# Performance work log

Hardware: AMD Instinct MI355X
Metric: run time of the kernel (lower is better)

Reference implementation:

```python
import jax, jax.numpy as jnp
import numpy as np

N = 60000      # nodes
E = 240000     # edges
H = 256        # hidden_channels
M = 64         # middle_channels
F1 = 12        # num_radial * num_spherical**2
F2 = 6         # num_radial * num_spherical
L = 4          # num_layers (InterBlocks)
NL = 3         # num_output_layers (residual linears per block)
G = 2000       # number of graphs in batch
EPS = 1e-5


def setup_inputs() -> dict:
    key = jax.random.key(0)
    ks = iter(jax.random.split(key, 64))
    def nrm(shape, scale=0.05):
        return jax.random.normal(next(ks), shape, jnp.float32) * scale
    inp = {
        'x_idx': jax.random.randint(next(ks), (N, 9), 0, 178, jnp.int32),
        'edge_attr_idx': jax.random.randint(next(ks), (E, 3), 0, 18, jnp.int32),
        'edge_index': jax.random.randint(next(ks), (2, E), 0, N, jnp.int32),
        'batch': jnp.sort(jax.random.randint(next(ks), (N,), 0, G, jnp.int32)),
        'feature1': jax.random.uniform(next(ks), (E, F1), jnp.float32),
        'feature2': jax.random.uniform(next(ks), (E, F2), jnp.float32),
        # embeddings
        'x_tab': nrm((178, H)), 'e_tab': nrm((18, H)),
        # lin_x: Linear + BN + ReLU
        'linx_w': nrm((L, H, H)), 'linx_b': jnp.zeros((L, H)), 'linx_g': jnp.ones((L, H)), 'linx_be': jnp.zeros((L, H)),
        # lin_feat1: Linear(F1,M) + BN(M) + ReLU + Linear(M,H) + ReLU
        'f1_w1': nrm((L, F1, M)), 'f1_b1': jnp.zeros((L, M)), 'f1_g': jnp.ones((L, M)), 'f1_be': jnp.zeros((L, M)),
        'f1_w2': nrm((L, M, H)), 'f1_b2': jnp.zeros((L, H)),
        # lin_feat2: Linear(F2,M) + BN(M) + ReLU + Linear(M,H) + ReLU
        'f2_w1': nrm((L, F2, M)), 'f2_b1': jnp.zeros((L, M)), 'f2_g': jnp.ones((L, M)), 'f2_be': jnp.zeros((L, M)),
        'f2_w2': nrm((L, M, H)), 'f2_b2': jnp.zeros((L, H)),
        # EdgeGraphConv 1 & 2 (PyG GraphConv: lin_rel(aggr) + lin_root(x), root has no bias)
        'c1_rel_w': nrm((L, H, H)), 'c1_rel_b': jnp.zeros((L, H)), 'c1_root_w': nrm((L, H, H)),
        'c2_rel_w': nrm((L, H, H)), 'c2_rel_b': jnp.zeros((L, H)), 'c2_root_w': nrm((L, H, H)),
        # lin_cat
        'cat_w': nrm((L, 2 * H, H)), 'cat_b': jnp.zeros((L, H)),
        # residual linears
        'lins_w': nrm((L, NL, H, H)), 'lins_b': jnp.zeros((L, NL, H)),
        # GraphNorm
        'gn_w': jnp.ones((L, H)), 'gn_b': jnp.zeros((L, H)), 'gn_ms': jnp.ones((L, H)),
        # final
        'fin_w': nrm((L, H, H)), 'fin_b': jnp.zeros((L, H)),
    }
    return inp


def _bn(h, g, b):
    m = h.mean(0)
    v = jnp.mean((h - m) ** 2, axis=0)
    return (h - m) * jax.lax.rsqrt(v + EPS) * g + b


def _conv(x, src, dst, ew, rel_w, rel_b, root_w):
    # EdgeGraphConv: message = x_j * edge_weight, sum-aggregate at dst
    msg = x[src] * ew                                   # [E, H]
    agg = jax.ops.segment_sum(msg, dst, num_segments=N)  # [N, H]
    return agg @ rel_w + rel_b + x @ root_w


def _graphnorm(h, batch, w, b, ms):
    cnt = jnp.maximum(jax.ops.segment_sum(jnp.ones((h.shape[0], 1), h.dtype), batch, num_segments=G), 1.0)
    mean = jax.ops.segment_sum(h, batch, num_segments=G) / cnt
    out = h - ms * mean[batch]
    var = jax.ops.segment_sum(out ** 2, batch, num_segments=G) / cnt
    return out * jax.lax.rsqrt(var[batch] + EPS) * w + b


def reference(x_idx, edge_attr_idx, edge_index, batch, feature1, feature2, x_tab, e_tab,
              linx_w, linx_b, linx_g, linx_be,
              f1_w1, f1_b1, f1_g, f1_be, f1_w2, f1_b2,
              f2_w1, f2_b1, f2_g, f2_be, f2_w2, f2_b2,
              c1_rel_w, c1_rel_b, c1_root_w, c2_rel_w, c2_rel_b, c2_root_w,
              cat_w, cat_b, lins_w, lins_b, gn_w, gn_b, gn_ms, fin_w, fin_b):
    relu = jax.nn.relu
    x = x_tab[x_idx].sum(1)                 # [N, H] atom-feature embedding sum
    _e = e_tab[edge_attr_idx].sum(1)        # edge embedding (computed, unused downstream as in source)
    src, dst = edge_index[0], edge_index[1]
    for l in range(L):
        xl = relu(_bn(x @ linx_w[l] + linx_b[l], linx_g[l], linx_be[l]))
        w1 = relu(relu(_bn(feature1 @ f1_w1[l] + f1_b1[l], f1_g[l], f1_be[l])) @ f1_w2[l] + f1_b2[l])
        w2 = relu(relu(_bn(feature2 @ f2_w1[l] + f2_b1[l], f2_g[l], f2_be[l])) @ f2_w2[l] + f2_b2[l])
        h1 = relu(_conv(xl, src, dst, w1, c1_rel_w[l], c1_rel_b[l], c1_root_w[l]))
        h2 = relu(_conv(xl, src, dst, w2, c2_rel_w[l], c2_rel_b[l], c2_root_w[l]))
        h = relu(jnp.concatenate([h1, h2], axis=1) @ cat_w[l] + cat_b[l])
        h = h + xl
        for k in range(NL):
            h = relu(h @ lins_w[l, k] + lins_b[l, k]) + h
        h = _graphnorm(h, batch, gn_w[l], gn_b[l], gn_ms[l])
        x = h @ fin_w[l] + fin_b[l]
    return x
```

## Files before the change

kernel.cpp:

```cpp
#include <hip/hip_runtime.h>
#include <cstdint>

constexpr int Nn = 60000;
constexpr int Ee = 240000;
constexpr int Hh = 256;
constexpr int Mm = 64;
constexpr int F1c = 12;
constexpr int Lc = 4;
constexpr int NLc = 3;
constexpr int Gc = 2000;
constexpr float EPSc = 1e-5f;
constexpr int NB = (Nn + 255) / 256;
constexpr int CSB = 256;

typedef _Float16 f16x8 __attribute__((ext_vector_type(8)));
typedef __attribute__((ext_vector_type(4))) float f32x4;
typedef __attribute__((ext_vector_type(4))) unsigned short u16x4;
typedef unsigned short ushortt;

__device__ __forceinline__ ushortt f2h(float f) {
    union { _Float16 h; ushortt u; } c; c.h = (_Float16)f; return c.u;
}
__device__ __forceinline__ float h2f(ushortt u) {
    union { _Float16 h; ushortt u; } c; c.u = u; return (float)c.h;
}

__global__ void embed_x_kernel(const int* __restrict__ xidx, const float* __restrict__ xtab,
                               ushortt* __restrict__ x) {
    int n = blockIdx.x;
    int c = threadIdx.x;
    __shared__ int idx[9];
    if (c < 9) idx[c] = xidx[n * 9 + c];
    __syncthreads();
    float s = 0.f;
#pragma unroll
    for (int j = 0; j < 9; j++) s += xtab[idx[j] * Hh + c];
    x[(size_t)n * Hh + c] = f2h(s);
}

__global__ void seg_bounds_kernel(const int* __restrict__ batch, int* __restrict__ gstart) {
    int g = blockIdx.x * 256 + threadIdx.x;
    if (g > Gc) return;
    if (g == Gc) { gstart[Gc] = Nn; return; }
    int lo = 0, hi = Nn;
    while (lo < hi) { int mid = (lo + hi) >> 1; if (batch[mid] < g) lo = mid + 1; else hi = mid; }
    gstart[g] = lo;
}

__global__ void deg_hist_kernel(const int* __restrict__ ei, int* __restrict__ deg) {
    int e = blockIdx.x * 256 + threadIdx.x;
    if (e >= Ee) return;
    atomicAdd(&deg[ei[Ee + e]], 1);
}

__global__ void psum_block_kernel(const int* __restrict__ deg, int* __restrict__ iscan,
                                  int* __restrict__ bsum) {
    __shared__ int s[256];
    int t = threadIdx.x;
    int i = blockIdx.x * 256 + t;
    int v = (i < Nn) ? deg[i] : 0;
    s[t] = v;
    __syncthreads();
    for (int off = 1; off < 256; off <<= 1) {
        int add = (t >= off) ? s[t - off] : 0;
        __syncthreads();
        s[t] += add;
        __syncthreads();
    }
    if (i < Nn) iscan[i] = s[t];
    if (t == 255) bsum[blockIdx.x] = s[255];
}

__global__ void scan_bsum_kernel(const int* __restrict__ bsum, int* __restrict__ ebase,
                                 int* __restrict__ rowptr) {
    if (threadIdx.x != 0 || blockIdx.x != 0) return;
    int run = 0;
    for (int b = 0; b < NB; b++) { ebase[b] = run; run += bsum[b]; }
    rowptr[Nn] = Ee;
}

__global__ void finalize_rowptr_kernel(const int* __restrict__ deg, const int* __restrict__ iscan,
                                       const int* __restrict__ ebase, int* __restrict__ rowptr) {
    int i = blockIdx.x * 256 + threadIdx.x;
    if (i >= Nn) return;
    rowptr[i] = ebase[i >> 8] + iscan[i] - deg[i];
}

__global__ void fill_eid_kernel(const int* __restrict__ ei, int* __restrict__ cursor,
                                int* __restrict__ eid, int* __restrict__ esrc) {
    int e = blockIdx.x * 256 + threadIdx.x;
    if (e >= Ee) return;
    int dst = ei[Ee + e];
    int pos = atomicAdd(&cursor[dst], 1);
    eid[pos] = e;
    esrc[pos] = ei[e];
}

template<int K>
__global__ void gather_feat_kernel(const float* __restrict__ F, const int* __restrict__ eid,
                                   ushortt* __restrict__ featS) {
    long i = (long)blockIdx.x * 256 + threadIdx.x;
    if (i >= (long)Ee * K) return;
    int e = (int)(i / K);
    int k = (int)(i % K);
    featS[i] = f2h(F[(size_t)eid[e] * K + k]);
}

__global__ void wconv_kernel(const float* __restrict__ src, ushortt* __restrict__ dst,
                             int nmat, int K, long dstMS, int kOff, long srcMS) {
    long idx = (long)blockIdx.x * 256 + threadIdx.x;
    long tot = (long)nmat * 256 * K;
    if (idx >= tot) return;
    int k = (int)(idx % K);
    long t = idx / K;
    int c = (int)(t & 255);
    int m = (int)(t >> 8);
    float w = src[m * srcMS + (long)k * 256 + c];
    int kg = kOff + k;
    int ks = kg >> 5;
    int k5 = kg & 31;
    int kpp = (((k5 & 15) >> 2) << 3) + (((k5 >> 4) & 1) << 2) + (k5 & 3);
    long o = m * dstMS + ((long)ks * 256 + c) * 32 + kpp;
    dst[o] = f2h(w);
}

template<int K>
__global__ void gram_kernel(const float* __restrict__ F, float* __restrict__ G,
                            float* __restrict__ s) {
    constexpr int NP = K * (K + 1) / 2;
    __shared__ float Ft[256 * K];
    int tid = threadIdx.x;
    int pi = 0, pj = 0;
    if (tid < NP) {
        int tt = tid;
        for (pi = 0; pi < K; pi++) { if (tt <= pi) { pj = tt; break; } tt -= (pi + 1); }
    }
    float acc = 0.f;
    int ntiles = (Ee + 255) / 256;
    for (int tile = blockIdx.x; tile < ntiles; tile += gridDim.x) {
        long r0 = (long)tile * 256;
        for (int idx = tid; idx < 256 * K; idx += 256) {
            long r = r0 + idx / K;
            Ft[idx] = (r < Ee) ? F[r * K + idx % K] : 0.f;
        }
        __syncthreads();
        if (tid < NP) {
            for (int r = 0; r < 256; r++) acc += Ft[r * K + pi] * Ft[r * K + pj];
        } else if (tid < NP + K) {
            int i = tid - NP;
            for (int r = 0; r < 256; r++) acc += Ft[r * K + i];
        }
        __syncthreads();
    }
    if (tid < NP) {
        atomicAdd(&G[pi * K + pj], acc);
        if (pi != pj) atomicAdd(&G[pj * K + pi], acc);
    } else if (tid < NP + K) {
        atomicAdd(&s[tid - NP], acc);
    }
}

__global__ void edge_bnparams_kernel(
    const float* __restrict__ G1, const float* __restrict__ s1,
    const float* __restrict__ G2, const float* __restrict__ s2,
    const float* __restrict__ f1_w1, const float* __restrict__ f1_b1,
    const float* __restrict__ f1_g, const float* __restrict__ f1_be,
    const float* __restrict__ f2_w1, const float* __restrict__ f2_b1,
    const float* __restrict__ f2_g, const float* __restrict__ f2_be,
    float Ecnt, float* __restrict__ scsAll, float* __restrict__ shsAll) {
    int lb = blockIdx.x;
    int l = lb >> 1, br = lb & 1;
    int m = threadIdx.x;
    const float* G = br ? G2 : G1;
    const float* sv = br ? s2 : s1;
    int K = br ? 6 : F1c;
    const float* W  = br ? (f2_w1 + (size_t)l * 6 * Mm)   : (f1_w1 + (size_t)l * F1c * Mm);
    const float* bb = br ? (f2_b1 + l * Mm) : (f1_b1 + l * Mm);
    const float* gg = br ? (f2_g + l * Mm)  : (f1_g + l * Mm);
    const float* be = br ? (f2_be + l * Mm) : (f1_be + l * Mm);
    float wm[F1c];
    for (int i = 0; i < K; i++) wm[i] = W[i * Mm + m];
    float sw = 0.f;
    for (int i = 0; i < K; i++) sw += sv[i] * wm[i];
    float q = 0.f;
    for (int i = 0; i < K; i++) {
        float gi = 0.f;
        for (int j = 0; j < K; j++) gi += G[i * K + j] * wm[j];
        q += wm[i] * gi;
    }
    float rinv = 1.f / Ecnt;
    float colsum = sw + Ecnt * bb[m];
    float colsq = q + 2.f * bb[m] * sw + Ecnt * bb[m] * bb[m];
    float mu = colsum * rinv;
    float var = colsq * rinv - mu * mu;
    float rs = rsqrtf(var + EPSc) * gg[m];
    scsAll[lb * 64 + m] = rs;
    shsAll[lb * 64 + m] = bb[m] * rs + be[m] - mu * rs;
}

__global__ void colstats_part_kernel(const ushortt* __restrict__ A, long tot4,
                                     float* __restrict__ part) {
    __shared__ float ls[1024], lq[1024];
    int tid = threadIdx.x;
    long i0 = (long)blockIdx.x * 256 + tid;
    long stride = (long)gridDim.x * 256;
    float s[4] = {0, 0, 0, 0}, q[4] = {0, 0, 0, 0};
    for (long i = i0; i < tot4; i += stride) {
        u16x4 v = *(const u16x4*)(A + i * 4);
#pragma unroll
        for (int j = 0; j < 4; j++) { float f = h2f(v[j]); s[j] += f; q[j] += f * f; }
    }
#pragma unroll
    for (int j = 0; j < 4; j++) { ls[tid * 4 + j] = s[j]; lq[tid * 4 + j] = q[j]; }
    __syncthreads();
    if (tid < 64) {
#pragma unroll
        for (int j = 0; j < 4; j++) {
            float ts = ls[tid * 4 + j] + ls[(tid + 64) * 4 + j] +
                       ls[(tid + 128) * 4 + j] + ls[(tid + 192) * 4 + j];
            float tq = lq[tid * 4 + j] + lq[(tid + 64) * 4 + j] +
                       lq[(tid + 128) * 4 + j] + lq[(tid + 192) * 4 + j];
            part[(size_t)blockIdx.x * 512 + tid * 4 + j] = ts;
            part[(size_t)blockIdx.x * 512 + 256 + tid * 4 + j] = tq;
        }
    }
}

__global__ void colstats_reduce_kernel(const float* __restrict__ part,
                                       float* __restrict__ colsum, float* __restrict__ colsq) {
    int t = blockIdx.x * 256 + threadIdx.x;
    float acc = 0.f;
    for (int b = 0; b < CSB; b++) acc += part[(size_t)b * 512 + t];
    if (t < 256) colsum[t] = acc;
    else colsq[t - 256] = acc;
}

__global__ void bn_relu_h_kernel(const ushortt* __restrict__ A, ushortt* __restrict__ outp,
                                 const float* __restrict__ sum, const float* __restrict__ sq,
                                 const float* __restrict__ g, const float* __restrict__ be,
                                 float rinv, long tot4) {
    long i = (long)blockIdx.x * 256 + threadIdx.x;
    if (i >= tot4) return;
    int c0 = (int)((i * 4) & 255);
    u16x4 v = *(const u16x4*)(A + i * 4);
    u16x4 o;
#pragma unroll
    for (int j = 0; j < 4; j++) {
        int c = c0 + j;
        float m = sum[c] * rinv;
        float var = sq[c] * rinv - m * m;
        float f = (h2f(v[j]) - m) * rsqrtf(var + EPSc) * g[c] + be[c];
        o[j] = f2h(fmaxf(f, 0.f));
    }
    *(u16x4*)(outp + i * 4) = o;
}

__global__ __launch_bounds__(256, 4) void bgemm_kernel(
    const void* __restrict__ A1v, int lda1, const ushortt* __restrict__ A2, int lda2,
    const ushortt* __restrict__ Wt,
    const float* __restrict__ bias, const ushortt* __restrict__ res,
    float* __restrict__ Cf, ushortt* __restrict__ Ch,
    int rows, int K1, int Ktot, int do_relu, int a1f32) {
    __shared__ char As[2][128 * 80];
    int tid = threadIdx.x;
    int lane = tid & 63;
    int wave = tid >> 6;
    int wrow0 = (wave >> 1) * 64;
    int wcol0 = (wave & 1) * 64;
    int r0 = blockIdx.y * 128;
    int j0 = blockIdx.x * 128;
    int l15 = lane & 15;
    int l4 = lane >> 4;

    int srow[4], sk4[4], soff[4];
#pragma unroll
    for (int p = 0; p < 4; p++) {
        int fid = p * 256 + tid;
        srow[p] = fid >> 3;
        sk4[p] = (fid & 7) * 4;
        soff[p] = srow[p] * 80 + ((((sk4[p] & 15) >> 2) << 4) + ((sk4[p] >> 4) << 3));
    }

    f32x4 acc[4][4];
#pragma unroll
    for (int i = 0; i < 4; i++)
#pragma unroll
        for (int j = 0; j < 4; j++) acc[i][j] = (f32x4){0.f, 0.f, 0.f, 0.f};

    for (int kt = 0; kt < Ktot; kt += 64) {
        const void* Av; int lda; int koff; int f32;
        if (kt < K1) { Av = A1v; lda = lda1; koff = kt; f32 = a1f32; }
        else         { Av = (const void*)A2; lda = lda2; koff = kt - K1; f32 = 0; }

        u16x4 hv[2][4];
        if (f32) {
#pragma unroll
            for (int h = 0; h < 2; h++)
#pragma unroll
                for (int p = 0; p < 4; p++) {
                    int rg = r0 + srow[p]; if (rg >= rows) rg = rows - 1;
                    float4 v = *(const float4*)((const float*)Av +
                        (size_t)rg * lda + koff + h * 32 + sk4[p]);
                    u16x4 hh;
                    hh[0] = f2h(v.x); hh[1] = f2h(v.y); hh[2] = f2h(v.z); hh[3] = f2h(v.w);
                    hv[h][p] = hh;
                }
        } else {
#pragma unroll
            for (int h = 0; h < 2; h++)
#pragma unroll
                for (int p = 0; p < 4; p++) {
                    int rg = r0 + srow[p]; if (rg >= rows) rg = rows - 1;
                    hv[h][p] = *(const u16x4*)((const ushortt*)Av +
                        (size_t)rg * lda + koff + h * 32 + sk4[p]);
                }
        }
        f16x8 bh[2][4];
#pragma unroll
        for (int h = 0; h < 2; h++) {
            long kb = ((long)((kt + h * 32) >> 5) * 256) * 32;
#pragma unroll
            for (int j = 0; j < 4; j++) {
                int colrow = j0 + wcol0 + j * 16 + l15;
                bh[h][j] = *(const f16x8*)(Wt + kb + (long)colrow * 32 + l4 * 8);
            }
        }
#pragma unroll
        for (int h = 0; h < 2; h++)
#pragma unroll
            for (int p = 0; p < 4; p++) *(u16x4*)(As[h] + soff[p]) = hv[h][p];
        __syncthreads();

#pragma unroll
        for (int h = 0; h < 2; h++) {
            f16x8 ah[4];
#pragma unroll
            for (int i = 0; i < 4; i++) {
                int row = wrow0 + i * 16 + l15;
                ah[i] = *(const f16x8*)(As[h] + row * 80 + l4 * 16);
            }
#pragma unroll
            for (int i = 0; i < 4; i++)
#pragma unroll
                for (int j = 0; j < 4; j++)
                    acc[i][j] = __builtin_amdgcn_mfma_f32_16x16x32_f16(ah[i], bh[h][j], acc[i][j], 0, 0, 0);
        }
        __syncthreads();
    }

#pragma unroll
    for (int i = 0; i < 4; i++) {
#pragma unroll
        for (int r = 0; r < 4; r++) {
            int row = r0 + wrow0 + i * 16 + l4 * 4 + r;
            if (row >= rows) continue;
#pragma unroll
            for (int j = 0; j < 4; j++) {
                int col = j0 + wcol0 + j * 16 + l15;
                float v = acc[i][j][r] + bias[col];
                if (do_relu) v = fmaxf(v, 0.f);
                if (res) v += h2f(res[(size_t)row * 256 + col]);
                if (Cf) Cf[(size_t)row * 256 + col] = v;
                if (Ch) Ch[(size_t)row * 256 + col] = f2h(v);
            }
        }
    }
}

template<int K>
__global__ __launch_bounds__(256, 4) void edge_gemm_kernel(
    const ushortt* __restrict__ featS, const float* __restrict__ W1,
    const float* __restrict__ scs, const float* __restrict__ shs,
    const ushortt* __restrict__ Wt, const float* __restrict__ bias,
    ushortt* __restrict__ Wc, int c0, int ec) {
    constexpr int KP = K + 1;
    __shared__ char As[2][128 * 80];
    __shared__ float Fs[128 * KP];
    __shared__ float W1s[K * 64];
    __shared__ float scsS[64], shsS[64];
    int tid = threadIdx.x;
    for (int i = tid; i < K * 64; i += 256) W1s[i] = W1[i];
    if (tid < 64) { scsS[tid] = scs[tid]; shsS[tid] = shs[tid]; }
    int r0 = blockIdx.y * 128;
    for (int idx = tid; idx < 128 * K; idx += 256) {
        int row = idx / K;
        int k = idx % K;
        long e = (long)c0 + r0 + row;
        if (e >= Ee) e = Ee - 1;
        Fs[row * KP + k] = h2f(featS[e * K + k]);
    }
    __syncthreads();
    {
        int row = tid >> 1;
        int m0 = (tid & 1) * 32;
        const float* fr = &Fs[row * KP];
#pragma unroll
        for (int mm = 0; mm < 32; mm++) {
            int m = m0 + mm;
            float u = 0.f;
#pragma unroll
            for (int k = 0; k < K; k++) u += fr[k] * W1s[k * 64 + m];
            float v = fmaxf(u * scsS[m] + shsS[m], 0.f);
            int k5 = m & 31;
            int kpp = (((k5 & 15) >> 2) << 3) + (((k5 >> 4) & 1) << 2) + (k5 & 3);
            *(ushortt*)(As[m >> 5] + row * 80 + kpp * 2) = f2h(v);
        }
    }
    __syncthreads();

    int lane = tid & 63;
    int wave = tid >> 6;
    int wrow0 = (wave >> 1) * 64;
    int wcol0 = (wave & 1) * 64;
    int j0 = blockIdx.x * 128;
    int l15 = lane & 15;
    int l4 = lane >> 4;

    f32x4 acc[4][4];
#pragma unroll
    for (int i = 0; i < 4; i++)
#pragma unroll
        for (int j = 0; j < 4; j++) acc[i][j] = (f32x4){0.f, 0.f, 0.f, 0.f};

#pragma unroll
    for (int kt = 0; kt < 64; kt += 32) {
        f16x8 bh[4];
        long kb = ((long)(kt >> 5) * 256) * 32;
#pragma unroll
        for (int j = 0; j < 4; j++) {
            int colrow = j0 + wcol0 + j * 16 + l15;
            bh[j] = *(const f16x8*)(Wt + kb + (long)colrow * 32 + l4 * 8);
        }
        f16x8 ah[4];
        const char* Az = As[kt >> 5];
#pragma unroll
        for (int i = 0; i < 4; i++) {
            int row = wrow0 + i * 16 + l15;
            ah[i] = *(const f16x8*)(Az + row * 80 + l4 * 16);
        }
#pragma unroll
        for (int i = 0; i < 4; i++)
#pragma unroll
            for (int j = 0; j < 4; j++)
                acc[i][j] = __builtin_amdgcn_mfma_f32_16x16x32_f16(ah[i], bh[j], acc[i][j], 0, 0, 0);
    }

#pragma unroll
    for (int i = 0; i < 4; i++) {
#pragma unroll
        for (int r = 0; r < 4; r++) {
            int row = wrow0 + i * 16 + l4 * 4 + r;
            if (r0 + row >= ec) continue;
#pragma unroll
            for (int j = 0; j < 4; j++) {
                int col = j0 + wcol0 + j * 16 + l15;
                float v = fmaxf(acc[i][j][r] + bias[col], 0.f);
                Wc[(size_t)(r0 + row) * 256 + col] = f2h(v);
            }
        }
    }
}

__global__ __launch_bounds__(256) void gather_agg_kernel(
    const int* __restrict__ rowptr, const int* __restrict__ esrc,
    const ushortt* __restrict__ Wc, const ushortt* __restrict__ xl,
    float* __restrict__ agg, ushortt* __restrict__ out16, int c0, int c1, int first) {
    int n = (blockIdx.x * 256 + threadIdx.x) >> 6;
    if (n >= Nn) return;
    int lane = threadIdx.x & 63;
    int rs = rowptr[n], re = rowptr[n + 1];
    if (rs < c0) rs = c0;
    if (re > c1) re = c1;
    float4 acc;
    if (out16 || first) {
        acc = make_float4(0.f, 0.f, 0.f, 0.f);
    } else {
        if (rs >= re) return;
        acc = *(float4*)(agg + (size_t)n * Hh + lane * 4);
    }
    for (int i = rs; i < re; i++) {
        u16x4 wv = *(const u16x4*)(Wc + (size_t)(i - c0) * Hh + lane * 4);
        u16x4 xv = *(const u16x4*)(xl + (size_t)esrc[i] * Hh + lane * 4);
        acc.x += h2f(wv[0]) * h2f(xv[0]);
        acc.y += h2f(wv[1]) * h2f(xv[1]);
        acc.z += h2f(wv[2]) * h2f(xv[2]);
        acc.w += h2f(wv[3]) * h2f(xv[3]);
    }
    if (out16) {
        u16x4 o;
        o[0] = f2h(acc.x); o[1] = f2h(acc.y); o[2] = f2h(acc.z); o[3] = f2h(acc.w);
        *(u16x4*)(out16 + (size_t)n * Hh + lane * 4) = o;
    } else {
        *(float4*)(agg + (size_t)n * Hh + lane * 4) = acc;
    }
}

__global__ __launch_bounds__(256) void gn_fused_kernel(
    const ushortt* __restrict__ h, const int* __restrict__ gstart,
    const float* __restrict__ ms, const float* __restrict__ w, const float* __restrict__ b,
    ushortt* __restrict__ outp) {
    __shared__ ushortt seg[128 * 256];
    int g = blockIdx.x;
    int c = threadIdx.x;
    int s = gstart[g], e = gstart[g + 1];
    int cnt = e - s;
    float cntf = (float)(cnt > 1 ? cnt : 1);
    float msc = ms[c], wc = w[c], bc = b[c];
    if (cnt <= 128) {
        float acc = 0.f;
        for (int n = 0; n < cnt; n++) {
            ushortt v = h[(size_t)(s + n) * Hh + c];
            seg[n * 256 + c] = v;
            acc += h2f(v);
        }
        float mean = acc / cntf;
        float sq = 0.f;
        for (int n = 0; n < cnt; n++) {
            ushortt ho = f2h(h2f(seg[n * 256 + c]) - msc * mean);
            seg[n * 256 + c] = ho;
            float o2 = h2f(ho);
            sq += o2 * o2;
        }
        float rstd = rsqrtf(sq / cntf + EPSc);
        for (int n = 0; n < cnt; n++) {
            float ov = h2f(seg[n * 256 + c]);
            outp[(size_t)(s + n) * Hh + c] = f2h(ov * rstd * wc + bc);
        }
    } else {
        float acc = 0.f;
        for (int n = s; n < e; n++) acc += h2f(h[(size_t)n * Hh + c]);
        float mean = acc / cntf;
        float sq = 0.f;
        for (int n = s; n < e; n++) {
            float ov = h2f(f2h(h2f(h[(size_t)n * Hh + c]) - msc * mean));
            sq += ov * ov;
        }
        float rstd = rsqrtf(sq / cntf + EPSc);
        for (int n = s; n < e; n++) {
            float ov = h2f(f2h(h2f(h[(size_t)n * Hh + c]) - msc * mean));
            outp[(size_t)n * Hh + c] = f2h(ov * rstd * wc + bc);
        }
    }
}

extern "C" void kernel_launch(void* const* d_in, const int* in_sizes, int n_in,
                              void* d_out, int out_size, void* d_ws, size_t ws_size,
                              hipStream_t stream) {
    const int* x_idx      = (const int*)d_in[0];
    const int* edge_index = (const int*)d_in[2];
    const int* batch      = (const int*)d_in[3];
    const float* feature1 = (const float*)d_in[4];
    const float* feature2 = (const float*)d_in[5];
    const float* x_tab    = (const float*)d_in[6];
    const float* linx_w   = (const float*)d_in[8];
    const float* linx_b   = (const float*)d_in[9];
    const float* linx_g   = (const float*)d_in[10];
    const float* linx_be  = (const float*)d_in[11];
    const float* f1_w1    = (const float*)d_in[12];
    const float* f1_b1    = (const float*)d_in[13];
    const float* f1_g     = (const float*)d_in[14];
    const float* f1_be    = (const float*)d_in[15];
    const float* f1_w2    = (const float*)d_in[16];
    const float* f1_b2    = (const float*)d_in[17];
    const float* f2_w1    = (const float*)d_in[18];
    const float* f2_b1    = (const float*)d_in[19];
    const float* f2_g     = (const float*)d_in[20];
    const float* f2_be    = (const float*)d_in[21];
    const float* f2_w2    = (const float*)d_in[22];
    const float* f2_b2    = (const float*)d_in[23];
    const float* c1_rel_w  = (const float*)d_in[24];
    const float* c1_rel_b  = (const float*)d_in[25];
    const float* c1_root_w = (const float*)d_in[26];
    const float* c2_rel_w  = (const float*)d_in[27];
    const float* c2_rel_b  = (const float*)d_in[28];
    const float* c2_root_w = (const float*)d_in[29];
    const float* cat_w    = (const float*)d_in[30];
    const float* cat_b    = (const float*)d_in[31];
    const float* lins_w   = (const float*)d_in[32];
    const float* lins_b   = (const float*)d_in[33];
    const float* gn_w     = (const float*)d_in[34];
    const float* gn_b     = (const float*)d_in[35];
    const float* gn_ms    = (const float*)d_in[36];
    const float* fin_w    = (const float*)d_in[37];
    const float* fin_b    = (const float*)d_in[38];

    size_t NH = (size_t)Nn * Hh;
    char* p = (char*)d_ws;
    ushortt* X  = (ushortt*)p; p += NH * 2;
    ushortt* B1 = (ushortt*)p; p += NH * 2;
    ushortt* B2 = (ushortt*)p; p += NH * 2;
    ushortt* B3 = (ushortt*)p; p += NH * 2;
    float* aggF = (float*)d_out;
    ushortt* aggH = (ushortt*)d_out;
    float* colsum = (float*)p; p += 256 * 4;
    float* colsq  = (float*)p; p += 256 * 4;
    float* part = (float*)p; p += (size_t)CSB * 512 * 4;
    float* G1 = (float*)p; p += 160 * 4;
    float* s1 = (float*)p; p += 16 * 4;
    float* G2 = (float*)p; p += 48 * 4;
    float* s2 = (float*)p; p += 16 * 4;
    float* scsAll = (float*)p; p += 8 * 64 * 4;
    float* shsAll = (float*)p; p += 8 * 64 * 4;
    int* gstart = (int*)p; p += 2048 * 4;
    int* deg    = (int*)p; p += Nn * 4;
    int* iscan  = (int*)p; p += Nn * 4;
    int* rowptr = (int*)p; p += (Nn + 256) * 4;
    int* cursor = (int*)p; p += Nn * 4;
    int* bsum   = (int*)p; p += 256 * 4;
    int* ebase  = (int*)p; p += 256 * 4;
    int* eid    = (int*)p; p += (size_t)Ee * 4;
    int* esrc   = (int*)p; p += (size_t)Ee * 4;
    ushortt* featS1 = (ushortt*)p; p += (size_t)Ee * F1c * 2;
    ushortt* featS2 = (ushortt*)p; p += (size_t)Ee * 6 * 2;
    ushortt* linxW = (ushortt*)p; p += (size_t)4 * 65536 * 2;
    ushortt* convW = (ushortt*)p; p += (size_t)16 * 65536 * 2;
    ushortt* catW  = (ushortt*)p; p += (size_t)8 * 65536 * 2;
    ushortt* linsW = (ushortt*)p; p += (size_t)12 * 65536 * 2;
    ushortt* finW  = (ushortt*)p; p += (size_t)4 * 65536 * 2;
    ushortt* fw2W  = (ushortt*)p; p += (size_t)8 * 16384 * 2;
    long availB = (long)ws_size - (long)(p - (char*)d_ws) - 1024;
    int CE = (int)(availB / (Hh * 2));
    if (CE > Ee) CE = Ee;
    if (CE < 8000) CE = 8000;
    ushortt* Wcb = (ushortt*)p;
    int single = (CE >= Ee) ? 1 : 0;

    long tot4 = (long)NH / 4;
    int blks4 = (int)((tot4 + 255) / 256);
    int blksE = (Ee + 255) / 256;
    int blksN = (Nn + 255) / 256;

    embed_x_kernel<<<Nn, 256, 0, stream>>>(x_idx, x_tab, X);
    seg_bounds_kernel<<<(Gc + 256) / 256, 256, 0, stream>>>(batch, gstart);
    hipMemsetAsync(deg, 0, Nn * sizeof(int), stream);
    deg_hist_kernel<<<blksE, 256, 0, stream>>>(edge_index, deg);
    psum_block_kernel<<<NB, 256, 0, stream>>>(deg, iscan, bsum);
    scan_bsum_kernel<<<1, 64, 0, stream>>>(bsum, ebase, rowptr);
    finalize_rowptr_kernel<<<blksN, 256, 0, stream>>>(deg, iscan, ebase, rowptr);
    hipMemcpyAsync(cursor, rowptr, Nn * sizeof(int), hipMemcpyDeviceToDevice, stream);
    fill_eid_kernel<<<blksE, 256, 0, stream>>>(edge_index, cursor, eid, esrc);
    gather_feat_kernel<F1c><<<(int)(((long)Ee * F1c + 255) / 256), 256, 0, stream>>>(
        feature1, eid, featS1);
    gather_feat_kernel<6><<<(int)(((long)Ee * 6 + 255) / 256), 256, 0, stream>>>(
        feature2, eid, featS2);

    hipMemsetAsync(G1, 0, 240 * sizeof(float), stream);
    gram_kernel<F1c><<<240, 256, 0, stream>>>(feature1, G1, s1);
    gram_kernel<6><<<240, 256, 0, stream>>>(feature2, G2, s2);
    edge_bnparams_kernel<<<8, 64, 0, stream>>>(G1, s1, G2, s2,
                                               f1_w1, f1_b1, f1_g, f1_be,
                                               f2_w1, f2_b1, f2_g, f2_be,
                                               (float)Ee, scsAll, shsAll);

    auto wcv = [&](const float* src, ushortt* dh, int nmat, int K,
                   long dstMS, int kOff, long srcMS) {
        long tot = (long)nmat * 256 * K;
        wconv_kernel<<<(int)((tot + 255) / 256), 256, 0, stream>>>(src, dh, nmat, K,
                                                                   dstMS, kOff, srcMS);
    };
    wcv(linx_w, linxW, 4, 256, 65536, 0, 65536);
    wcv(c1_rel_w,  convW,          4, 256, 262144, 0,   65536);
    wcv(c1_root_w, convW,          4, 256, 262144, 256, 65536);
    wcv(c2_rel_w,  convW + 131072, 4, 256, 262144, 0,   65536);
    wcv(c2_root_w, convW + 131072, 4, 256, 262144, 256, 65536);
    wcv(cat_w, catW, 4, 512, 131072, 0, 131072);
    wcv(lins_w, linsW, 12, 256, 65536, 0, 65536);
    wcv(fin_w, finW, 4, 256, 65536, 0, 65536);
    wcv(f1_w2, fw2W,         4, 64, 32768, 0, 16384);
    wcv(f2_w2, fw2W + 16384, 4, 64, 32768, 0, 16384);

    dim3 gN(2, (Nn + 127) / 128);

    for (int l = 0; l < Lc; l++) {
        bgemm_kernel<<<gN, 256, 0, stream>>>(X, 256, nullptr, 0,
                                             linxW + (size_t)l * 65536,
                                             linx_b + l * Hh, nullptr, nullptr, B1,
                                             Nn, 256, 256, 0, 0);
        colstats_part_kernel<<<CSB, 256, 0, stream>>>(B1, tot4, part);
        colstats_reduce_kernel<<<2, 256, 0, stream>>>(part, colsum, colsq);
        bn_relu_h_kernel<<<blks4, 256, 0, stream>>>(B1, X, colsum, colsq,
                                                    linx_g + l * Hh, linx_be + l * Hh,
                                                    1.f / Nn, tot4);

        for (int br = 0; br < 2; br++) {
            const float* fw1 = br == 0 ? f1_w1 + (size_t)l * F1c * Mm : f2_w1 + (size_t)l * 6 * Mm;
            const float* fb2 = br == 0 ? f1_b2 + l * Hh : f2_b2 + l * Hh;
            const float* relb = br == 0 ? c1_rel_b + l * Hh : c2_rel_b + l * Hh;
            ushortt* fw2t = fw2W + (size_t)l * 32768 + (br ? 16384 : 0);
            ushortt* cvt  = convW + (size_t)l * 262144 + (br ? 131072 : 0);
            ushortt* hbr = br == 0 ? B3 : B2;
            const float* scsP = scsAll + (l * 2 + br) * 64;
            const float* shsP = shsAll + (l * 2 + br) * 64;

            for (int c0 = 0; c0 < Ee; c0 += CE) {
                int ec = Ee - c0 < CE ? Ee - c0 : CE;
                dim3 gc(2, (ec + 127) / 128);
                if (br == 0)
                    edge_gemm_kernel<F1c><<<gc, 256, 0, stream>>>(
                        featS1, fw1, scsP, shsP, fw2t, fb2, Wcb, c0, ec);
                else
                    edge_gemm_kernel<6><<<gc, 256, 0, stream>>>(
                        featS2, fw1, scsP, shsP, fw2t, fb2, Wcb, c0, ec);
                gather_agg_kernel<<<(Nn * 64 + 255) / 256, 256, 0, stream>>>(
                    rowptr, esrc, Wcb, X, aggF, single ? aggH : nullptr,
                    c0, c0 + ec, c0 == 0 ? 1 : 0);
            }
            if (single)
                bgemm_kernel<<<gN, 256, 0, stream>>>(aggH, 256, X, 256, cvt,
                                                     relb, nullptr, nullptr, hbr,
                                                     Nn, 256, 512, 1, 0);
            else
                bgemm_kernel<<<gN, 256, 0, stream>>>(aggF, 256, X, 256, cvt,
                                                     relb, nullptr, nullptr, hbr,
                                                     Nn, 256, 512, 1, 1);
        }

        bgemm_kernel<<<gN, 256, 0, stream>>>(B3, 256, B2, 256,
                                             catW + (size_t)l * 131072,
                                             cat_b + l * Hh, X, nullptr, B1,
                                             Nn, 256, 512, 1, 0);
        ushortt* cur = B1; ushortt* oth = B2;
        for (int k = 0; k < NLc; k++) {
            bgemm_kernel<<<gN, 256, 0, stream>>>(cur, 256, nullptr, 0,
                                                 linsW + ((size_t)l * NLc + k) * 65536,
                                                 lins_b + ((size_t)l * NLc + k) * Hh, cur,
                                                 nullptr, oth, Nn, 256, 256, 1, 0);
            ushortt* t = cur; cur = oth; oth = t;
        }
        gn_fused_kernel<<<Gc, 256, 0, stream>>>(cur, gstart, gn_ms + l * Hh,
                                                gn_w + l * Hh, gn_b + l * Hh, oth);
        bgemm_kernel<<<gN, 256, 0, stream>>>(oth, 256, nullptr, 0,
                                             finW + (size_t)l * 65536,
                                             fin_b + l * Hh, nullptr,
                                             (l == Lc - 1) ? (float*)d_out : nullptr,
                                             (l == Lc - 1) ? nullptr : X,
                                             Nn, 256, 256, 0, 0);
    }
}
```

Before: 2.675 ms.

## Fuse edge MLP GEMM with CSR segmented aggregation via per-block run sums

```diff
diff --git a/kernel.cpp b/kernel.cpp
--- a/kernel.cpp
+++ b/kernel.cpp
@@ -87,13 +87,15 @@
 }
 
 __global__ void fill_eid_kernel(const int* __restrict__ ei, int* __restrict__ cursor,
-                                int* __restrict__ eid, int* __restrict__ esrc) {
+                                int* __restrict__ eid, int* __restrict__ esrc,
+                                int* __restrict__ dstS) {
     int e = blockIdx.x * 256 + threadIdx.x;
     if (e >= Ee) return;
     int dst = ei[Ee + e];
     int pos = atomicAdd(&cursor[dst], 1);
     eid[pos] = e;
     esrc[pos] = ei[e];
+    dstS[pos] = dst;
 }
 
 template<int K>
@@ -367,25 +369,47 @@
     }
 }
 
+__global__ __launch_bounds__(256) void agg_init_kernel(const int* __restrict__ rowptr,
+                                                       float* __restrict__ agg) {
+    int n = (blockIdx.x * 256 + threadIdx.x) >> 6;
+    if (n >= Nn) return;
+    int lane = threadIdx.x & 63;
+    int rs = rowptr[n], re = rowptr[n + 1];
+    bool need = (rs == re) || ((rs >> 6) != ((re - 1) >> 6));
+    if (!need) return;
+    f32x4 z = (f32x4){0.f, 0.f, 0.f, 0.f};
+    *(f32x4*)(agg + (size_t)n * Hh + lane * 4) = z;
+}
+
 template<int K>
-__global__ __launch_bounds__(256, 4) void edge_gemm_kernel(
+__global__ __launch_bounds__(256, 2) void edge_fused_kernel(
     const ushortt* __restrict__ featS, const float* __restrict__ W1,
     const float* __restrict__ scs, const float* __restrict__ shs,
     const ushortt* __restrict__ Wt, const float* __restrict__ bias,
-    ushortt* __restrict__ Wc, int c0, int ec) {
+    const int* __restrict__ rowptr, const int* __restrict__ esrcS,
+    const int* __restrict__ dstS, const ushortt* __restrict__ xl,
+    float* __restrict__ agg) {
     constexpr int KP = K + 1;
     __shared__ char As[2][128 * 80];
     __shared__ float Fs[128 * KP];
     __shared__ float W1s[K * 64];
     __shared__ float scsS[64], shsS[64];
+    __shared__ ushortt wt[128 * 130];
+    __shared__ int edstL[128], esrcL[128];
     int tid = threadIdx.x;
+    int e0 = blockIdx.y * 128;
     for (int i = tid; i < K * 64; i += 256) W1s[i] = W1[i];
     if (tid < 64) { scsS[tid] = scs[tid]; shsS[tid] = shs[tid]; }
-    int r0 = blockIdx.y * 128;
+    if (tid < 128) {
+        long e = (long)e0 + tid;
+        if (e >= Ee) e = Ee - 1;
+        edstL[tid] = dstS[e];
+        esrcL[tid] = esrcS[e];
+    }
     for (int idx = tid; idx < 128 * K; idx += 256) {
         int row = idx / K;
         int k = idx % K;
-        long e = (long)c0 + r0 + row;
+        long e = (long)e0 + row;
         if (e >= Ee) e = Ee - 1;
         Fs[row * KP + k] = h2f(featS[e * K + k]);
     }
@@ -446,52 +470,45 @@
     }
 
 #pragma unroll
-    for (int i = 0; i < 4; i++) {
+    for (int i = 0; i < 4; i++)
 #pragma unroll
         for (int r = 0; r < 4; r++) {
             int row = wrow0 + i * 16 + l4 * 4 + r;
-            if (r0 + row >= ec) continue;
 #pragma unroll
             for (int j = 0; j < 4; j++) {
-                int col = j0 + wcol0 + j * 16 + l15;
-                float v = fmaxf(acc[i][j][r] + bias[col], 0.f);
-                Wc[(size_t)(r0 + row) * 256 + col] = f2h(v);
+                int col = wcol0 + j * 16 + l15;
+                float v = fmaxf(acc[i][j][r] + bias[j0 + col], 0.f);
+                wt[row * 130 + col] = f2h(v);
             }
         }
-    }
-}
-
-__global__ __launch_bounds__(256) void gather_agg_kernel(
-    const int* __restrict__ rowptr, const int* __restrict__ esrc,
-    const ushortt* __restrict__ Wc, const ushortt* __restrict__ xl,
-    float* __restrict__ agg, ushortt* __restrict__ out16, int c0, int c1, int first) {
-    int n = (blockIdx.x * 256 + threadIdx.x) >> 6;
-    if (n >= Nn) return;
-    int lane = threadIdx.x & 63;
-    int rs = rowptr[n], re = rowptr[n + 1];
-    if (rs < c0) rs = c0;
-    if (re > c1) re = c1;
-    float4 acc;
-    if (out16 || first) {
-        acc = make_float4(0.f, 0.f, 0.f, 0.f);
-    } else {
-        if (rs >= re) return;
-        acc = *(float4*)(agg + (size_t)n * Hh + lane * 4);
-    }
-    for (int i = rs; i < re; i++) {
-        u16x4 wv = *(const u16x4*)(Wc + (size_t)(i - c0) * Hh + lane * 4);
-        u16x4 xv = *(const u16x4*)(xl + (size_t)esrc[i] * Hh + lane * 4);
-        acc.x += h2f(wv[0]) * h2f(xv[0]);
-        acc.y += h2f(wv[1]) * h2f(xv[1]);
-        acc.z += h2f(wv[2]) * h2f(xv[2]);
-        acc.w += h2f(wv[3]) * h2f(xv[3]);
-    }
-    if (out16) {
-        u16x4 o;
-        o[0] = f2h(acc.x); o[1] = f2h(acc.y); o[2] = f2h(acc.z); o[3] = f2h(acc.w);
-        *(u16x4*)(out16 + (size_t)n * Hh + lane * 4) = o;
-    } else {
-        *(float4*)(agg + (size_t)n * Hh + lane * 4) = acc;
+    __syncthreads();
+
+    int col = tid & 127;
+    int rb = (tid >> 7) * 64;
+    float run = 0.f;
+    int prevd = -1;
+    for (int r = rb; r < rb + 64; r++) {
+        if (e0 + r >= Ee) break;
+        int d = edstL[r];
+        if (d != prevd) {
+            if (prevd >= 0) {
+                int rs = rowptr[prevd], re = rowptr[prevd + 1];
+                float* ap = agg + (size_t)prevd * Hh + j0 + col;
+                if ((rs >> 6) == ((re - 1) >> 6)) *ap = run;
+                else atomicAdd(ap, run);
+            }
+            run = 0.f;
+            prevd = d;
+        }
+        float w = h2f(wt[r * 130 + col]);
+        float xv = h2f(xl[(size_t)esrcL[r] * Hh + j0 + col]);
+        run += w * xv;
+    }
+    if (prevd >= 0) {
+        int rs = rowptr[prevd], re = rowptr[prevd + 1];
+        float* ap = agg + (size_t)prevd * Hh + j0 + col;
+        if ((rs >> 6) == ((re - 1) >> 6)) *ap = run;
+        else atomicAdd(ap, run);
     }
 }
 
@@ -591,7 +608,6 @@
     ushortt* B2 = (ushortt*)p; p += NH * 2;
     ushortt* B3 = (ushortt*)p; p += NH * 2;
     float* aggF = (float*)d_out;
-    ushortt* aggH = (ushortt*)d_out;
     float* colsum = (float*)p; p += 256 * 4;
     float* colsq  = (float*)p; p += 256 * 4;
     float* part = (float*)p; p += (size_t)CSB * 512 * 4;
@@ -610,6 +626,7 @@
     int* ebase  = (int*)p; p += 256 * 4;
     int* eid    = (int*)p; p += (size_t)Ee * 4;
     int* esrc   = (int*)p; p += (size_t)Ee * 4;
+    int* dstS   = (int*)p; p += (size_t)Ee * 4;
     ushortt* featS1 = (ushortt*)p; p += (size_t)Ee * F1c * 2;
     ushortt* featS2 = (ushortt*)p; p += (size_t)Ee * 6 * 2;
     ushortt* linxW = (ushortt*)p; p += (size_t)4 * 65536 * 2;
@@ -618,12 +635,6 @@
     ushortt* linsW = (ushortt*)p; p += (size_t)12 * 65536 * 2;
     ushortt* finW  = (ushortt*)p; p += (size_t)4 * 65536 * 2;
     ushortt* fw2W  = (ushortt*)p; p += (size_t)8 * 16384 * 2;
-    long availB = (long)ws_size - (long)(p - (char*)d_ws) - 1024;
-    int CE = (int)(availB / (Hh * 2));
-    if (CE > Ee) CE = Ee;
-    if (CE < 8000) CE = 8000;
-    ushortt* Wcb = (ushortt*)p;
-    int single = (CE >= Ee) ? 1 : 0;
 
     long tot4 = (long)NH / 4;
     int blks4 = (int)((tot4 + 255) / 256);
@@ -638,7 +649,7 @@
     scan_bsum_kernel<<<1, 64, 0, stream>>>(bsum, ebase, rowptr);
     finalize_rowptr_kernel<<<blksN, 256, 0, stream>>>(deg, iscan, ebase, rowptr);
     hipMemcpyAsync(cursor, rowptr, Nn * sizeof(int), hipMemcpyDeviceToDevice, stream);
-    fill_eid_kernel<<<blksE, 256, 0, stream>>>(edge_index, cursor, eid, esrc);
+    fill_eid_kernel<<<blksE, 256, 0, stream>>>(edge_index, cursor, eid, esrc, dstS);
     gather_feat_kernel<F1c><<<(int)(((long)Ee * F1c + 255) / 256), 256, 0, stream>>>(
         feature1, eid, featS1);
     gather_feat_kernel<6><<<(int)(((long)Ee * 6 + 255) / 256), 256, 0, stream>>>(
@@ -670,6 +681,7 @@
     wcv(f2_w2, fw2W + 16384, 4, 64, 32768, 0, 16384);
 
     dim3 gN(2, (Nn + 127) / 128);
+    dim3 gE(2, (Ee + 127) / 128);
 
     for (int l = 0; l < Lc; l++) {
         bgemm_kernel<<<gN, 256, 0, stream>>>(X, 256, nullptr, 0,
@@ -692,27 +704,17 @@
             const float* scsP = scsAll + (l * 2 + br) * 64;
             const float* shsP = shsAll + (l * 2 + br) * 64;
 
-            for (int c0 = 0; c0 < Ee; c0 += CE) {
-                int ec = Ee - c0 < CE ? Ee - c0 : CE;
-                dim3 gc(2, (ec + 127) / 128);
-                if (br == 0)
-                    edge_gemm_kernel<F1c><<<gc, 256, 0, stream>>>(
-                        featS1, fw1, scsP, shsP, fw2t, fb2, Wcb, c0, ec);
-                else
-                    edge_gemm_kernel<6><<<gc, 256, 0, stream>>>(
-                        featS2, fw1, scsP, shsP, fw2t, fb2, Wcb, c0, ec);
-                gather_agg_kernel<<<(Nn * 64 + 255) / 256, 256, 0, stream>>>(
-                    rowptr, esrc, Wcb, X, aggF, single ? aggH : nullptr,
-                    c0, c0 + ec, c0 == 0 ? 1 : 0);
-            }
-            if (single)
-                bgemm_kernel<<<gN, 256, 0, stream>>>(aggH, 256, X, 256, cvt,
-                                                     relb, nullptr, nullptr, hbr,
-                                                     Nn, 256, 512, 1, 0);
+            agg_init_kernel<<<(Nn * 64 + 255) / 256, 256, 0, stream>>>(rowptr, aggF);
+            if (br == 0)
+                edge_fused_kernel<F1c><<<gE, 256, 0, stream>>>(
+                    featS1, fw1, scsP, shsP, fw2t, fb2, rowptr, esrc, dstS, X, aggF);
             else
-                bgemm_kernel<<<gN, 256, 0, stream>>>(aggF, 256, X, 256, cvt,
-                                                     relb, nullptr, nullptr, hbr,
-                                                     Nn, 256, 512, 1, 1);
+                edge_fused_kernel<6><<<gE, 256, 0, stream>>>(
+                    featS2, fw1, scsP, shsP, fw2t, fb2, rowptr, esrc, dstS, X, aggF);
+
+            bgemm_kernel<<<gN, 256, 0, stream>>>(aggF, 256, X, 256, cvt,
+                                                 relb, nullptr, nullptr, hbr,
+                                                 Nn, 256, 512, 1, 1);
         }
 
         bgemm_kernel<<<gN, 256, 0, stream>>>(B3, 256, B2, 256,
```

Result: slower. 3.856 ms (+44.2%).
